# Kernel tuning notes

Hardware: AMD Instinct MI355X
Metric: run time of the kernel (lower is better)

The kernel has to match this reference:

```python
import jax, jax.numpy as jnp
import numpy as np

SOBEL_X = jnp.array([[1., 0., -1.], [2., 0., -2.], [1., 0., -1.]], dtype=jnp.float32).reshape(1, 1, 3, 3)
SOBEL_Y = jnp.array([[1., 2., 1.], [0., 0., 0.], [-1., -2., -1.]], dtype=jnp.float32).reshape(1, 1, 3, 3)
EPS = 1e-3


def _sobel(img, kern):
    # img: [N, 1, H, W]; 3x3 conv, zero padding 1 (torch Conv2d padding=1)
    return jax.lax.conv_general_dilated(
        img, kern, window_strides=(1, 1), padding='SAME',
        dimension_numbers=('NCHW', 'OIHW', 'NCHW'))


def _compute_flow(frames):
    # frames: [B, T, 3, H, W] -> flow: [B, T-1, 2, H, W]
    B, T, C, H, W = frames.shape
    gray = (0.2989 * frames[:, :, 0] + 0.587 * frames[:, :, 1]
            + 0.114 * frames[:, :, 2])  # [B, T, H, W]
    I1 = gray[:, :-1].reshape(B * (T - 1), 1, H, W)
    I2 = gray[:, 1:].reshape(B * (T - 1), 1, H, W)
    Ix = _sobel(I1, SOBEL_X)
    Iy = _sobel(I1, SOBEL_Y)
    It = I2 - I1
    denom = Ix * Ix + Iy * Iy + EPS
    u = -Ix * It / denom
    v = -Iy * It / denom
    return jnp.concatenate([u, v], axis=1).reshape(B, T - 1, 2, H, W)


def setup_inputs() -> dict:
    key = jax.random.key(0)
    k1, k2 = jax.random.split(key)
    shape = (8, 8, 3, 256, 256)  # [B, T, C, H, W]
    pred = jax.random.uniform(k1, shape, dtype=jnp.float32)
    gt = jax.random.uniform(k2, shape, dtype=jnp.float32)
    return {"pred": pred, "gt": gt}


def reference(pred, gt):
    pred_flow = _compute_flow(pred)  # [B, T-1, 2, H, W]
    gt_flow = _compute_flow(gt)
    # motion magnitude: mean abs frame diff over channels, broadcast over 2 flow channels
    motion_mag = jnp.abs(gt[:, 1:] - gt[:, :-1]).mean(axis=2, keepdims=True)  # [B, T-1, 1, H, W]
    flow_loss = (jnp.abs(pred_flow - gt_flow) * motion_mag).mean()
    return flow_loss
```

## Files before the change

kernel.cpp:

```cpp
#include <hip/hip_runtime.h>

#define BB 8
#define TT 8
#define HH 256
#define WW 256
#define FRAME_PIX (HH * WW)
#define XW 128
#define RROWS 8
#define NYT (HH / RROWS)
#define NXT (WW / XW)
#define PADW 136
#define NBLK (BB * 2 * NYT * NXT)
#define EPS 1e-3f
#define INV_N (1.0f / (float)((size_t)BB * (TT - 1) * 2 * HH * WW))

__device__ __forceinline__ float4 ld4(const float* __restrict__ p) {
    return *reinterpret_cast<const float4*>(p);
}
__device__ __forceinline__ void st4(float* p, const float4 v) {
    *reinterpret_cast<float4*>(p) = v;
}
__device__ __forceinline__ float4 gray4(const float4 r, const float4 g, const float4 b) {
    float4 o;
    o.x = 0.2989f * r.x + 0.587f * g.x + 0.114f * b.x;
    o.y = 0.2989f * r.y + 0.587f * g.y + 0.114f * b.y;
    o.z = 0.2989f * r.z + 0.587f * g.z + 0.114f * b.z;
    o.w = 0.2989f * r.w + 0.587f * g.w + 0.114f * b.w;
    return o;
}

__global__ __launch_bounds__(256, 4) void flow_loss_kernel(
    const float* __restrict__ pred, const float* __restrict__ gt,
    float* __restrict__ partial)
{
    __shared__ float gbuf[2][RROWS + 2][PADW];

    const int ytile = blockIdx.x >> 1;
    const int xtile = blockIdx.x & 1;
    const int half  = blockIdx.y;
    const int b     = blockIdx.z;
    const int t0    = half * 4;
    const int tend  = t0 + (half ? 3 : 4);
    const int y0    = ytile * RROWS;
    const int x0    = xtile * XW;
    const int tid   = threadIdx.x;
    const size_t fs = (size_t)3 * FRAME_PIX;
    const float* pb = pred + (size_t)b * TT * fs;
    const float* gb = gt   + (size_t)b * TT * fs;

    const int r  = tid >> 5;
    const int cx = (tid & 31) * 4;
    const size_t coff = (size_t)(y0 + r) * WW + (x0 + cx);

    bool e_act = false, e_val = false;
    int  e_img = 0;
    size_t e_off = 0;
    float* e_dst = &gbuf[0][0][0];
    if (tid < 128) {
        e_act = true;
        e_img = tid >> 6;
        const int rsel = (tid >> 5) & 1;
        const int ec   = (tid & 31) * 4;
        const int ey   = rsel ? (y0 + RROWS) : (y0 - 1);
        e_val = (unsigned)ey < HH;
        e_off = e_val ? ((size_t)ey * WW + x0 + ec) : 0;
        e_dst = &gbuf[e_img][rsel ? RROWS + 1 : 0][4 + ec];
    } else if (tid < 168) {
        const int j = tid - 128;
        e_act = true;
        e_img = j / 20;
        const int rem  = j % 20;
        const int side = rem / 10;
        const int prow = rem % 10;
        const int ey = y0 - 1 + prow;
        const int ex = side ? (x0 + XW) : (x0 - 4);
        e_val = ((unsigned)ey < HH) && ((unsigned)ex < WW);
        e_off = e_val ? ((size_t)ey * WW + ex) : 0;
        e_dst = &gbuf[e_img][prow][side ? 4 + XW : 0];
    }

    float4 p2c[3], g2c[3], ecur[3];
    float  mmc[4];

    {
        const float* p1 = pb + (size_t)t0 * fs;
        const float* g1 = gb + (size_t)t0 * fs;
        const float4 pr  = ld4(p1 + coff);
        const float4 pg  = ld4(p1 + coff + FRAME_PIX);
        const float4 pbl = ld4(p1 + coff + 2 * FRAME_PIX);
        const float4 a0  = ld4(g1 + coff);
        const float4 a1  = ld4(g1 + coff + FRAME_PIX);
        const float4 a2  = ld4(g1 + coff + 2 * FRAME_PIX);
        const float* eb0 = e_img ? g1 : p1;
        float4 x0v = make_float4(0.f,0.f,0.f,0.f), x1v = x0v, x2v = x0v;
        if (e_act && e_val) {
            x0v = ld4(eb0 + e_off);
            x1v = ld4(eb0 + e_off + FRAME_PIX);
            x2v = ld4(eb0 + e_off + 2 * FRAME_PIX);
        }
        const float* p2 = p1 + fs;
        const float* g2 = g1 + fs;
        p2c[0] = ld4(p2 + coff);
        p2c[1] = ld4(p2 + coff + FRAME_PIX);
        p2c[2] = ld4(p2 + coff + 2 * FRAME_PIX);
        g2c[0] = ld4(g2 + coff);
        g2c[1] = ld4(g2 + coff + FRAME_PIX);
        g2c[2] = ld4(g2 + coff + 2 * FRAME_PIX);
        const float* eb1 = e_img ? g2 : p2;
        ecur[0] = make_float4(0.f,0.f,0.f,0.f); ecur[1] = ecur[0]; ecur[2] = ecur[0];
        if (e_act && e_val) {
            ecur[0] = ld4(eb1 + e_off);
            ecur[1] = ld4(eb1 + e_off + FRAME_PIX);
            ecur[2] = ld4(eb1 + e_off + 2 * FRAME_PIX);
        }
        st4(&gbuf[0][r + 1][4 + cx], gray4(pr, pg, pbl));
        st4(&gbuf[1][r + 1][4 + cx], gray4(a0, a1, a2));
        if (e_act) st4(e_dst, gray4(x0v, x1v, x2v));
        mmc[0] = (fabsf(g2c[0].x - a0.x) + fabsf(g2c[1].x - a1.x) + fabsf(g2c[2].x - a2.x)) * (1.f/3.f);
        mmc[1] = (fabsf(g2c[0].y - a0.y) + fabsf(g2c[1].y - a1.y) + fabsf(g2c[2].y - a2.y)) * (1.f/3.f);
        mmc[2] = (fabsf(g2c[0].z - a0.z) + fabsf(g2c[1].z - a1.z) + fabsf(g2c[2].z - a2.z)) * (1.f/3.f);
        mmc[3] = (fabsf(g2c[0].w - a0.w) + fabsf(g2c[1].w - a1.w) + fabsf(g2c[2].w - a2.w)) * (1.f/3.f);
    }
    __syncthreads();

    float s = 0.f;
    for (int t = t0; t < tend; ++t) {
        const bool more = (t + 1 < tend);

        float4 p2n[3], g2n[3], en[3];
        if (more) {
            const float* p3 = pb + (size_t)(t + 2) * fs;
            const float* g3 = gb + (size_t)(t + 2) * fs;
            p2n[0] = ld4(p3 + coff);
            p2n[1] = ld4(p3 + coff + FRAME_PIX);
            p2n[2] = ld4(p3 + coff + 2 * FRAME_PIX);
            g2n[0] = ld4(g3 + coff);
            g2n[1] = ld4(g3 + coff + FRAME_PIX);
            g2n[2] = ld4(g3 + coff + 2 * FRAME_PIX);
            const float* eb = e_img ? g3 : p3;
            en[0] = make_float4(0.f,0.f,0.f,0.f); en[1] = en[0]; en[2] = en[0];
            if (e_act && e_val) {
                en[0] = ld4(eb + e_off);
                en[1] = ld4(eb + e_off + FRAME_PIX);
                en[2] = ld4(eb + e_off + 2 * FRAME_PIX);
            }
        }

        const float4 gp2 = gray4(p2c[0], p2c[1], p2c[2]);
        const float4 gg2 = gray4(g2c[0], g2c[1], g2c[2]);

        float up[4], vp[4];
        #pragma unroll
        for (int img = 0; img < 2; ++img) {
            float w0[6], w1[6], w2[6];
            {
                const float* p = &gbuf[img][r][cx];
                const float4 A = ld4(p), B = ld4(p + 4), C = ld4(p + 8);
                w0[0] = A.w; w0[1] = B.x; w0[2] = B.y; w0[3] = B.z; w0[4] = B.w; w0[5] = C.x;
            }
            {
                const float* p = &gbuf[img][r + 1][cx];
                const float4 A = ld4(p), B = ld4(p + 4), C = ld4(p + 8);
                w1[0] = A.w; w1[1] = B.x; w1[2] = B.y; w1[3] = B.z; w1[4] = B.w; w1[5] = C.x;
            }
            {
                const float* p = &gbuf[img][r + 2][cx];
                const float4 A = ld4(p), B = ld4(p + 4), C = ld4(p + 8);
                w2[0] = A.w; w2[1] = B.x; w2[2] = B.y; w2[3] = B.z; w2[4] = B.w; w2[5] = C.x;
            }
            const float4 gr2 = img ? gg2 : gp2;
            const float g2a[4] = {gr2.x, gr2.y, gr2.z, gr2.w};
            #pragma unroll
            for (int j = 0; j < 4; ++j) {
                const float Ix = (w0[j] - w0[j + 2]) + 2.0f * (w1[j] - w1[j + 2]) + (w2[j] - w2[j + 2]);
                const float Iy = (w0[j] + 2.0f * w0[j + 1] + w0[j + 2])
                               - (w2[j] + 2.0f * w2[j + 1] + w2[j + 2]);
                const float It = g2a[j] - w1[j + 1];
                const float inv = 1.0f / (Ix * Ix + Iy * Iy + EPS);
                if (img == 0) {
                    up[j] = -(Ix * It) * inv;
                    vp[j] = -(Iy * It) * inv;
                } else {
                    s += (fabsf(up[j] + (Ix * It) * inv) + fabsf(vp[j] + (Iy * It) * inv)) * mmc[j];
                }
            }
        }

        if (more) {
            float mmn[4];
            mmn[0] = (fabsf(g2n[0].x - g2c[0].x) + fabsf(g2n[1].x - g2c[1].x) + fabsf(g2n[2].x - g2c[2].x)) * (1.f/3.f);
            mmn[1] = (fabsf(g2n[0].y - g2c[0].y) + fabsf(g2n[1].y - g2c[1].y) + fabsf(g2n[2].y - g2c[2].y)) * (1.f/3.f);
            mmn[2] = (fabsf(g2n[0].z - g2c[0].z) + fabsf(g2n[1].z - g2c[1].z) + fabsf(g2n[2].z - g2c[2].z)) * (1.f/3.f);
            mmn[3] = (fabsf(g2n[0].w - g2c[0].w) + fabsf(g2n[1].w - g2c[1].w) + fabsf(g2n[2].w - g2c[2].w)) * (1.f/3.f);

            __syncthreads();
            st4(&gbuf[0][r + 1][4 + cx], gp2);
            st4(&gbuf[1][r + 1][4 + cx], gg2);
            if (e_act) st4(e_dst, gray4(ecur[0], ecur[1], ecur[2]));
            #pragma unroll
            for (int k = 0; k < 3; ++k) {
                p2c[k] = p2n[k];
                g2c[k] = g2n[k];
                ecur[k] = en[k];
            }
            mmc[0] = mmn[0]; mmc[1] = mmn[1]; mmc[2] = mmn[2]; mmc[3] = mmn[3];
            __syncthreads();
        }
    }

    #pragma unroll
    for (int off = 32; off > 0; off >>= 1) s += __shfl_down(s, off, 64);

    __shared__ float wsum[4];
    if ((tid & 63) == 0) wsum[tid >> 6] = s;
    __syncthreads();
    if (tid == 0) {
        partial[(b * 2 + half) * (NYT * NXT) + blockIdx.x] =
            wsum[0] + wsum[1] + wsum[2] + wsum[3];
    }
}

__global__ __launch_bounds__(256) void reduce_kernel(
    const float* __restrict__ partial, float* __restrict__ out)
{
    const float4 v = ld4(partial + threadIdx.x * 4);
    float s = (v.x + v.y) + (v.z + v.w);
    #pragma unroll
    for (int off = 32; off > 0; off >>= 1) s += __shfl_down(s, off, 64);

    __shared__ float wsum[4];
    if ((threadIdx.x & 63) == 0) wsum[threadIdx.x >> 6] = s;
    __syncthreads();
    if (threadIdx.x == 0) {
        out[0] = (wsum[0] + wsum[1] + wsum[2] + wsum[3]) * INV_N;
    }
}

extern "C" void kernel_launch(void* const* d_in, const int* in_sizes, int n_in,
                              void* d_out, int out_size, void* d_ws, size_t ws_size,
                              hipStream_t stream) {
    const float* pred = (const float*)d_in[0];
    const float* gt   = (const float*)d_in[1];
    float* partial    = (float*)d_ws;
    float* out        = (float*)d_out;

    dim3 grid(NYT * NXT, 2, BB);
    dim3 block(256);
    flow_loss_kernel<<<grid, block, 0, stream>>>(pred, gt, partial);
    reduce_kernel<<<1, 256, 0, stream>>>(partial, out);
}
```

Baseline: 121.4 us.

## Assign one frame pair per block instead of streaming over time

Measured after the change: 134.1 us. 1.1x slower.

```diff
diff --git a/kernel.cpp b/kernel.cpp
--- a/kernel.cpp
+++ b/kernel.cpp
@@ -2,6 +2,7 @@
 
 #define BB 8
 #define TT 8
+#define NPAIR (TT - 1)
 #define HH 256
 #define WW 256
 #define FRAME_PIX (HH * WW)
@@ -10,9 +11,9 @@
 #define NYT (HH / RROWS)
 #define NXT (WW / XW)
 #define PADW 136
-#define NBLK (BB * 2 * NYT * NXT)
+#define NBLK (NYT * NXT * NPAIR * BB)
 #define EPS 1e-3f
-#define INV_N (1.0f / (float)((size_t)BB * (TT - 1) * 2 * HH * WW))
+#define INV_N (1.0f / (float)((size_t)BB * NPAIR * 2 * HH * WW))
 
 __device__ __forceinline__ float4 ld4(const float* __restrict__ p) {
     return *reinterpret_cast<const float4*>(p);
@@ -29,7 +30,7 @@
     return o;
 }
 
-__global__ __launch_bounds__(256, 4) void flow_loss_kernel(
+__global__ __launch_bounds__(256, 8) void flow_loss_kernel(
     const float* __restrict__ pred, const float* __restrict__ gt,
     float* __restrict__ partial)
 {
@@ -37,16 +38,16 @@
 
     const int ytile = blockIdx.x >> 1;
     const int xtile = blockIdx.x & 1;
-    const int half  = blockIdx.y;
+    const int t     = blockIdx.y;
     const int b     = blockIdx.z;
-    const int t0    = half * 4;
-    const int tend  = t0 + (half ? 3 : 4);
     const int y0    = ytile * RROWS;
     const int x0    = xtile * XW;
     const int tid   = threadIdx.x;
     const size_t fs = (size_t)3 * FRAME_PIX;
-    const float* pb = pred + (size_t)b * TT * fs;
-    const float* gb = gt   + (size_t)b * TT * fs;
+    const float* p1 = pred + (size_t)b * TT * fs + (size_t)t * fs;
+    const float* g1 = gt   + (size_t)b * TT * fs + (size_t)t * fs;
+    const float* p2 = p1 + fs;
+    const float* g2 = g1 + fs;
 
     const int r  = tid >> 5;
     const int cx = (tid & 31) * 4;
@@ -79,132 +80,76 @@
         e_dst = &gbuf[e_img][prow][side ? 4 + XW : 0];
     }
 
-    float4 p2c[3], g2c[3], ecur[3];
-    float  mmc[4];
+    const float4 a1r = ld4(p1 + coff);
+    const float4 a1g = ld4(p1 + coff + FRAME_PIX);
+    const float4 a1b = ld4(p1 + coff + 2 * FRAME_PIX);
+    const float4 b1r = ld4(g1 + coff);
+    const float4 b1g = ld4(g1 + coff + FRAME_PIX);
+    const float4 b1b = ld4(g1 + coff + 2 * FRAME_PIX);
+    const float4 a2r = ld4(p2 + coff);
+    const float4 a2g = ld4(p2 + coff + FRAME_PIX);
+    const float4 a2b = ld4(p2 + coff + 2 * FRAME_PIX);
+    const float4 b2r = ld4(g2 + coff);
+    const float4 b2g = ld4(g2 + coff + FRAME_PIX);
+    const float4 b2b = ld4(g2 + coff + 2 * FRAME_PIX);
+    float4 e0 = make_float4(0.f, 0.f, 0.f, 0.f), e1 = e0, e2 = e0;
+    if (e_act && e_val) {
+        const float* eb = e_img ? g1 : p1;
+        e0 = ld4(eb + e_off);
+        e1 = ld4(eb + e_off + FRAME_PIX);
+        e2 = ld4(eb + e_off + 2 * FRAME_PIX);
+    }
 
-    {
-        const float* p1 = pb + (size_t)t0 * fs;
-        const float* g1 = gb + (size_t)t0 * fs;
-        const float4 pr  = ld4(p1 + coff);
-        const float4 pg  = ld4(p1 + coff + FRAME_PIX);
-        const float4 pbl = ld4(p1 + coff + 2 * FRAME_PIX);
-        const float4 a0  = ld4(g1 + coff);
-        const float4 a1  = ld4(g1 + coff + FRAME_PIX);
-        const float4 a2  = ld4(g1 + coff + 2 * FRAME_PIX);
-        const float* eb0 = e_img ? g1 : p1;
-        float4 x0v = make_float4(0.f,0.f,0.f,0.f), x1v = x0v, x2v = x0v;
-        if (e_act && e_val) {
-            x0v = ld4(eb0 + e_off);
-            x1v = ld4(eb0 + e_off + FRAME_PIX);
-            x2v = ld4(eb0 + e_off + 2 * FRAME_PIX);
-        }
-        const float* p2 = p1 + fs;
-        const float* g2 = g1 + fs;
-        p2c[0] = ld4(p2 + coff);
-        p2c[1] = ld4(p2 + coff + FRAME_PIX);
-        p2c[2] = ld4(p2 + coff + 2 * FRAME_PIX);
-        g2c[0] = ld4(g2 + coff);
-        g2c[1] = ld4(g2 + coff + FRAME_PIX);
-        g2c[2] = ld4(g2 + coff + 2 * FRAME_PIX);
-        const float* eb1 = e_img ? g2 : p2;
-        ecur[0] = make_float4(0.f,0.f,0.f,0.f); ecur[1] = ecur[0]; ecur[2] = ecur[0];
-        if (e_act && e_val) {
-            ecur[0] = ld4(eb1 + e_off);
-            ecur[1] = ld4(eb1 + e_off + FRAME_PIX);
-            ecur[2] = ld4(eb1 + e_off + 2 * FRAME_PIX);
-        }
-        st4(&gbuf[0][r + 1][4 + cx], gray4(pr, pg, pbl));
-        st4(&gbuf[1][r + 1][4 + cx], gray4(a0, a1, a2));
-        if (e_act) st4(e_dst, gray4(x0v, x1v, x2v));
-        mmc[0] = (fabsf(g2c[0].x - a0.x) + fabsf(g2c[1].x - a1.x) + fabsf(g2c[2].x - a2.x)) * (1.f/3.f);
-        mmc[1] = (fabsf(g2c[0].y - a0.y) + fabsf(g2c[1].y - a1.y) + fabsf(g2c[2].y - a2.y)) * (1.f/3.f);
-        mmc[2] = (fabsf(g2c[0].z - a0.z) + fabsf(g2c[1].z - a1.z) + fabsf(g2c[2].z - a2.z)) * (1.f/3.f);
-        mmc[3] = (fabsf(g2c[0].w - a0.w) + fabsf(g2c[1].w - a1.w) + fabsf(g2c[2].w - a2.w)) * (1.f/3.f);
-    }
+    st4(&gbuf[0][r + 1][4 + cx], gray4(a1r, a1g, a1b));
+    st4(&gbuf[1][r + 1][4 + cx], gray4(b1r, b1g, b1b));
+    if (e_act) st4(e_dst, gray4(e0, e1, e2));
+
+    float mm[4];
+    mm[0] = (fabsf(b2r.x - b1r.x) + fabsf(b2g.x - b1g.x) + fabsf(b2b.x - b1b.x)) * (1.f / 3.f);
+    mm[1] = (fabsf(b2r.y - b1r.y) + fabsf(b2g.y - b1g.y) + fabsf(b2b.y - b1b.y)) * (1.f / 3.f);
+    mm[2] = (fabsf(b2r.z - b1r.z) + fabsf(b2g.z - b1g.z) + fabsf(b2b.z - b1b.z)) * (1.f / 3.f);
+    mm[3] = (fabsf(b2r.w - b1r.w) + fabsf(b2g.w - b1g.w) + fabsf(b2b.w - b1b.w)) * (1.f / 3.f);
+
+    const float4 gp2 = gray4(a2r, a2g, a2b);
+    const float4 gg2 = gray4(b2r, b2g, b2b);
+
     __syncthreads();
 
     float s = 0.f;
-    for (int t = t0; t < tend; ++t) {
-        const bool more = (t + 1 < tend);
-
-        float4 p2n[3], g2n[3], en[3];
-        if (more) {
-            const float* p3 = pb + (size_t)(t + 2) * fs;
-            const float* g3 = gb + (size_t)(t + 2) * fs;
-            p2n[0] = ld4(p3 + coff);
-            p2n[1] = ld4(p3 + coff + FRAME_PIX);
-            p2n[2] = ld4(p3 + coff + 2 * FRAME_PIX);
-            g2n[0] = ld4(g3 + coff);
-            g2n[1] = ld4(g3 + coff + FRAME_PIX);
-            g2n[2] = ld4(g3 + coff + 2 * FRAME_PIX);
-            const float* eb = e_img ? g3 : p3;
-            en[0] = make_float4(0.f,0.f,0.f,0.f); en[1] = en[0]; en[2] = en[0];
-            if (e_act && e_val) {
-                en[0] = ld4(eb + e_off);
-                en[1] = ld4(eb + e_off + FRAME_PIX);
-                en[2] = ld4(eb + e_off + 2 * FRAME_PIX);
+    float up[4], vp[4];
+    #pragma unroll
+    for (int img = 0; img < 2; ++img) {
+        float w0[6], w1[6], w2[6];
+        {
+            const float* p = &gbuf[img][r][cx];
+            const float4 A = ld4(p), B = ld4(p + 4), C = ld4(p + 8);
+            w0[0] = A.w; w0[1] = B.x; w0[2] = B.y; w0[3] = B.z; w0[4] = B.w; w0[5] = C.x;
+        }
+        {
+            const float* p = &gbuf[img][r + 1][cx];
+            const float4 A = ld4(p), B = ld4(p + 4), C = ld4(p + 8);
+            w1[0] = A.w; w1[1] = B.x; w1[2] = B.y; w1[3] = B.z; w1[4] = B.w; w1[5] = C.x;
+        }
+        {
+            const float* p = &gbuf[img][r + 2][cx];
+            const float4 A = ld4(p), B = ld4(p + 4), C = ld4(p + 8);
+            w2[0] = A.w; w2[1] = B.x; w2[2] = B.y; w2[3] = B.z; w2[4] = B.w; w2[5] = C.x;
+        }
+        const float4 gr2 = img ? gg2 : gp2;
+        const float g2a[4] = {gr2.x, gr2.y, gr2.z, gr2.w};
+        #pragma unroll
+        for (int j = 0; j < 4; ++j) {
+            const float Ix = (w0[j] - w0[j + 2]) + 2.0f * (w1[j] - w1[j + 2]) + (w2[j] - w2[j + 2]);
+            const float Iy = (w0[j] + 2.0f * w0[j + 1] + w0[j + 2])
+                           - (w2[j] + 2.0f * w2[j + 1] + w2[j + 2]);
+            const float It = g2a[j] - w1[j + 1];
+            const float inv = 1.0f / (Ix * Ix + Iy * Iy + EPS);
+            if (img == 0) {
+                up[j] = -(Ix * It) * inv;
+                vp[j] = -(Iy * It) * inv;
+            } else {
+                s += (fabsf(up[j] + (Ix * It) * inv) + fabsf(vp[j] + (Iy * It) * inv)) * mm[j];
             }
-        }
-
-        const float4 gp2 = gray4(p2c[0], p2c[1], p2c[2]);
-        const float4 gg2 = gray4(g2c[0], g2c[1], g2c[2]);
-
-        float up[4], vp[4];
-        #pragma unroll
-        for (int img = 0; img < 2; ++img) {
-            float w0[6], w1[6], w2[6];
-            {
-                const float* p = &gbuf[img][r][cx];
-                const float4 A = ld4(p), B = ld4(p + 4), C = ld4(p + 8);
-                w0[0] = A.w; w0[1] = B.x; w0[2] = B.y; w0[3] = B.z; w0[4] = B.w; w0[5] = C.x;
-            }
-            {
-                const float* p = &gbuf[img][r + 1][cx];
-                const float4 A = ld4(p), B = ld4(p + 4), C = ld4(p + 8);
-                w1[0] = A.w; w1[1] = B.x; w1[2] = B.y; w1[3] = B.z; w1[4] = B.w; w1[5] = C.x;
-            }
-            {
-                const float* p = &gbuf[img][r + 2][cx];
-                const float4 A = ld4(p), B = ld4(p + 4), C = ld4(p + 8);
-                w2[0] = A.w; w2[1] = B.x; w2[2] = B.y; w2[3] = B.z; w2[4] = B.w; w2[5] = C.x;
-            }
-            const float4 gr2 = img ? gg2 : gp2;
-            const float g2a[4] = {gr2.x, gr2.y, gr2.z, gr2.w};
-            #pragma unroll
-            for (int j = 0; j < 4; ++j) {
-                const float Ix = (w0[j] - w0[j + 2]) + 2.0f * (w1[j] - w1[j + 2]) + (w2[j] - w2[j + 2]);
-                const float Iy = (w0[j] + 2.0f * w0[j + 1] + w0[j + 2])
-                               - (w2[j] + 2.0f * w2[j + 1] + w2[j + 2]);
-                const float It = g2a[j] - w1[j + 1];
-                const float inv = 1.0f / (Ix * Ix + Iy * Iy + EPS);
-                if (img == 0) {
-                    up[j] = -(Ix * It) * inv;
-                    vp[j] = -(Iy * It) * inv;
-                } else {
-                    s += (fabsf(up[j] + (Ix * It) * inv) + fabsf(vp[j] + (Iy * It) * inv)) * mmc[j];
-                }
-            }
-        }
-
-        if (more) {
-            float mmn[4];
-            mmn[0] = (fabsf(g2n[0].x - g2c[0].x) + fabsf(g2n[1].x - g2c[1].x) + fabsf(g2n[2].x - g2c[2].x)) * (1.f/3.f);
-            mmn[1] = (fabsf(g2n[0].y - g2c[0].y) + fabsf(g2n[1].y - g2c[1].y) + fabsf(g2n[2].y - g2c[2].y)) * (1.f/3.f);
-            mmn[2] = (fabsf(g2n[0].z - g2c[0].z) + fabsf(g2n[1].z - g2c[1].z) + fabsf(g2n[2].z - g2c[2].z)) * (1.f/3.f);
-            mmn[3] = (fabsf(g2n[0].w - g2c[0].w) + fabsf(g2n[1].w - g2c[1].w) + fabsf(g2n[2].w - g2c[2].w)) * (1.f/3.f);
-
-            __syncthreads();
-            st4(&gbuf[0][r + 1][4 + cx], gp2);
-            st4(&gbuf[1][r + 1][4 + cx], gg2);
-            if (e_act) st4(e_dst, gray4(ecur[0], ecur[1], ecur[2]));
-            #pragma unroll
-            for (int k = 0; k < 3; ++k) {
-                p2c[k] = p2n[k];
-                g2c[k] = g2n[k];
-                ecur[k] = en[k];
-            }
-            mmc[0] = mmn[0]; mmc[1] = mmn[1]; mmc[2] = mmn[2]; mmc[3] = mmn[3];
-            __syncthreads();
         }
     }
 
@@ -215,12 +160,12 @@
     if ((tid & 63) == 0) wsum[tid >> 6] = s;
     __syncthreads();
     if (tid == 0) {
-        partial[(b * 2 + half) * (NYT * NXT) + blockIdx.x] =
+        partial[((b * NPAIR) + t) * (NYT * NXT) + blockIdx.x] =
             wsum[0] + wsum[1] + wsum[2] + wsum[3];
     }
 }
 
-__global__ __launch_bounds__(256) void reduce_kernel(
+__global__ __launch_bounds__(896) void reduce_kernel(
     const float* __restrict__ partial, float* __restrict__ out)
 {
     const float4 v = ld4(partial + threadIdx.x * 4);
@@ -228,11 +173,14 @@
     #pragma unroll
     for (int off = 32; off > 0; off >>= 1) s += __shfl_down(s, off, 64);
 
-    __shared__ float wsum[4];
+    __shared__ float wsum[14];
     if ((threadIdx.x & 63) == 0) wsum[threadIdx.x >> 6] = s;
     __syncthreads();
     if (threadIdx.x == 0) {
-        out[0] = (wsum[0] + wsum[1] + wsum[2] + wsum[3]) * INV_N;
+        float tot = 0.f;
+        #pragma unroll
+        for (int i = 0; i < 14; ++i) tot += wsum[i];
+        out[0] = tot * INV_N;
     }
 }
 
@@ -244,8 +192,8 @@
     float* partial    = (float*)d_ws;
     float* out        = (float*)d_out;
 
-    dim3 grid(NYT * NXT, 2, BB);
+    dim3 grid(NYT * NXT, NPAIR, BB);
     dim3 block(256);
     flow_loss_kernel<<<grid, block, 0, stream>>>(pred, gt, partial);
-    reduce_kernel<<<1, 256, 0, stream>>>(partial, out);
+    reduce_kernel<<<1, 896, 0, stream>>>(partial, out);
 }
```
